# Kernel optimization log

Hardware: AMD Instinct MI355X
Metric: run time of the kernel (lower is better)

Reference implementation:

```python
import jax, jax.numpy as jnp
import numpy as np

DT = 600.0          # init kwarg: dt (seconds)
STEPS = 48          # init kwarg: steps
R_EARTH = 6371000.0
DEG2RAD = np.pi / 180.0


def setup_inputs() -> dict:
    key = jax.random.key(0)
    k1, k2, k3 = jax.random.split(key, 3)
    B, H, W = 8, 1024, 1024
    T = jax.random.normal(k1, (B, H, W), jnp.float32)
    ug = 0.5 * jax.random.normal(k2, (B, H, W), jnp.float32)
    vg = 0.5 * jax.random.normal(k3, (B, H, W), jnp.float32)
    lat = jnp.linspace(20.0, 60.0, H, dtype=jnp.float32)   # degrees, matches repo linspace(20,60,nx)
    lon = jnp.linspace(100.0, 150.0, W, dtype=jnp.float32)  # degrees, matches repo linspace(100,150,ny)
    mask = jnp.ones((H, W), jnp.float32)
    return {"T": T, "ug": ug, "vg": vg, "lat": lat, "lon": lon, "mask": mask}


def reference(T, ug, vg, lat, lon, mask):
    dtype = T.dtype
    dlat = lat[1] - lat[0]
    dlon = lon[1] - lon[0]
    dy = R_EARTH * DEG2RAD * dlat                        # scalar
    # dx depends only on latitude (row): shape (H,1) -> broadcast (1,H,1)
    dx = (R_EARTH * DEG2RAD * dlon) * jnp.cos(lat * DEG2RAD)[:, None]
    dx_b = dx[None]                                       # (1,H,1)
    m = mask[None]                                        # (1,H,W)
    kernel = (jnp.array([[1., 2., 1.], [2., 4., 2.], [1., 2., 1.]], dtype) / 16.0).reshape(1, 1, 3, 3)

    def deriv_y(Tc):  # centered interior, one-sided edges along H (axis 1)
        mid = (Tc[:, 2:] - Tc[:, :-2]) / (2.0 * dy)
        top = (Tc[:, 1:2] - Tc[:, 0:1]) / dy
        bot = (Tc[:, -1:] - Tc[:, -2:-1]) / dy
        return jnp.concatenate([top, mid, bot], axis=1)

    def deriv_x(Tc):  # centered interior, one-sided edges along W (axis 2); dx is W-independent
        mid = (Tc[:, :, 2:] - Tc[:, :, :-2]) / (2.0 * dx_b)
        left = (Tc[:, :, 1:2] - Tc[:, :, 0:1]) / dx_b
        right = (Tc[:, :, -1:] - Tc[:, :, -2:-1]) / dx_b
        return jnp.concatenate([left, mid, right], axis=2)

    def smooth(x):  # 3x3 binomial filter, SAME (zero) padding, then mask
        y = jax.lax.conv_general_dilated(
            x[:, None], kernel, window_strides=(1, 1), padding=((1, 1), (1, 1)),
            dimension_numbers=("NCHW", "OIHW", "NCHW"))
        return y[:, 0] * m

    def step(Tc, _):
        Fc = -(ug * deriv_x(Tc) + vg * deriv_y(Tc)) * m   # masked advective tendency
        Tn = smooth(Tc + DT * Fc)
        return Tn, None

    T_final, _ = jax.lax.scan(step, T, None, length=STEPS)
    return T_final
```

## Files before the change

kernel.cpp:

```cpp
#include <hip/hip_runtime.h>


#define DEG2RAD 0.017453292519943295f
#define R_EARTH 6371000.0f
#define DT_S 600.0f

constexpr int NT    = 256;
constexpr int STRIP = 8;
constexpr int WPW   = 256;

__global__ __launch_bounds__(256)
void prep_kernel(const float* __restrict__ lat, const float* __restrict__ lon,
                 float* __restrict__ coef, int H) {
    int h = blockIdx.x * blockDim.x + threadIdx.x;
    if (h < H) {
        float dlon = lon[1] - lon[0];
        coef[h] = 1.0f / (R_EARTH * DEG2RAD * dlon * cosf(lat[h] * DEG2RAD));
    }
    if (h == 0) {
        float dlat = lat[1] - lat[0];
        coef[H] = 1.0f / (R_EARTH * DEG2RAD * dlat);
    }
}

constexpr int FWAVES = 4;
constexpr int SH3    = 8;
constexpr int NITER3 = SH3 + 10;

__global__ __launch_bounds__(256, 2)
void fused3_kernel(const float* __restrict__ Tin, const float* __restrict__ ug,
                   const float* __restrict__ vg, const float* __restrict__ mask,
                   const float* __restrict__ coef, float* __restrict__ Tout,
                   int H, int W) {
    const int lane = threadIdx.x & 63;
    const int wv   = threadIdx.x >> 6;
    const int h0   = blockIdx.x * SH3;
    const int b    = blockIdx.y;
    const int gw   = (wv << 8) + (lane << 2);
    const size_t plane = (size_t)H * W;
    const float* __restrict__ Tb  = Tin + b * plane;
    const float* __restrict__ ugb = ug  + b * plane;
    const float* __restrict__ vgb = vg  + b * plane;
    float* __restrict__ To = Tout + b * plane;
    const float inv_dy = coef[H];
    const bool isL = (lane == 0), isR = (lane == 63);
    const bool domL = (wv == 0), domR = (wv == FWAVES - 1);

    __shared__ float eT [8][FWAVES][2];
    __shared__ float eA1[8][FWAVES][2];
    __shared__ float eS1[8][FWAVES][2];
    __shared__ float eA2[8][FWAVES][2];
    __shared__ float eS2[8][FWAVES][2];
    __shared__ float eA3[8][FWAVES][2];

    auto rowc = [&](int r) { return min(max(r, 0), H - 1); };
    auto ld4 = [&](const float* __restrict__ p, int r) -> float4 {
        return *(const float4*)(p + (size_t)rowc(r) * W + gw);
    };
    const float4 z4 = make_float4(0.f, 0.f, 0.f, 0.f);

    float4 t0 = z4;
    float4 t1 = ld4(Tb, h0 - 6);
    float4 t2 = ld4(Tb, h0 - 5);
    float4 t3 = ld4(Tb, h0 - 4);
    float4 u0 = ld4(ugb, h0 - 5), u1 = z4, u2 = z4, u3 = z4, u4 = z4, u5 = z4;
    float4 g0 = ld4(vgb, h0 - 5), g1 = z4, g2 = z4, g3 = z4, g4 = z4, g5 = z4;
    float4 m0 = ld4(mask, h0 - 5), m1 = z4, m2 = z4, m3 = z4, m4 = z4, m5 = z4, m6 = z4;
    float4 a1p = z4, a1c = z4, a1n = z4;
    float4 s1p = z4, s1c = z4, s1n = z4;
    float4 a2p = z4, a2c = z4, a2n = z4;
    float4 s2p = z4, s2c = z4, s2n = z4;
    float4 a3p = z4, a3c = z4, a3n = z4;

    if (isL) { eT[3][wv][0] = t2.x; eT[4][wv][0] = t3.x; }
    if (isR) { eT[3][wv][1] = t2.w; eT[4][wv][1] = t3.w; }
    asm volatile("s_waitcnt lgkmcnt(0)" ::: "memory");
    __builtin_amdgcn_s_barrier();

    #pragma unroll
    for (int j = 0; j < NITER3; ++j) {
        const int a = h0 - 5 + j;
        const int rg_a1p = (j + 4) & 7;
        const int rg_a   = (j + 3) & 7;
        const int rg_am1 = (j + 2) & 7;
        const int rg_am2 = (j + 1) & 7;
        const int rg_am3 = (j + 0) & 7;
        const int rg_am4 = (j + 7) & 7;
        const int rg_am5 = (j + 6) & 7;
        const int rg_am6 = (j + 5) & 7;

        t0 = t1; t1 = t2; t2 = t3; t3 = ld4(Tb, a + 2);
        u5 = u4; u4 = u3; u3 = u2; u2 = u1; u1 = u0; u0 = ld4(ugb, a + 1);
        g5 = g4; g4 = g3; g3 = g2; g2 = g1; g1 = g0; g0 = ld4(vgb, a + 1);
        m6 = m5; m5 = m4; m4 = m3; m3 = m2; m2 = m1; m1 = m0; m0 = ld4(mask, a + 1);

        if (isL) eT[rg_a1p][wv][0] = t2.x;
        if (isR) eT[rg_a1p][wv][1] = t2.w;

        float4 a1_new = z4;
        if (a >= 0 && a < H) {
            const float ix  = coef[a];
            const float sy  = (a == 0 || a == H - 1) ? inv_dy : 0.5f * inv_dy;
            const float sxh = 0.5f * ix;
            float cL = __shfl_up(t1.w, 1);
            float cR = __shfl_down(t1.x, 1);
            float sxx = sxh, sxw = sxh;
            if (isL) { if (domL) { cL = t1.x; sxx = ix; } else cL = eT[rg_a][wv - 1][1]; }
            if (isR) { if (domR) { cR = t1.w; sxw = ix; } else cR = eT[rg_a][wv + 1][0]; }
            a1_new.x = t1.x + DT_S * (-(u1.x * ((t1.y - cL ) * sxx) + g1.x * ((t2.x - t0.x) * sy)) * m1.x);
            a1_new.y = t1.y + DT_S * (-(u1.y * ((t1.z - t1.x) * sxh) + g1.y * ((t2.y - t0.y) * sy)) * m1.y);
            a1_new.z = t1.z + DT_S * (-(u1.z * ((t1.w - t1.y) * sxh) + g1.z * ((t2.z - t0.z) * sy)) * m1.z);
            a1_new.w = t1.w + DT_S * (-(u1.w * ((cR  - t1.z) * sxw) + g1.w * ((t2.w - t0.w) * sy)) * m1.w);
        }
        if (isL) eA1[rg_a][wv][0] = a1_new.x;
        if (isR) eA1[rg_a][wv][1] = a1_new.w;
        a1n = a1_new;

        asm volatile("s_waitcnt lgkmcnt(0)" ::: "memory");
        __builtin_amdgcn_s_barrier();

        float4 s1_new = z4;
        if (j >= 2) {
            const int s = a - 1;
            if (s >= 0 && s < H) {
                float4 v;
                v.x = a1p.x + 2.f * a1c.x + a1n.x;
                v.y = a1p.y + 2.f * a1c.y + a1n.y;
                v.z = a1p.z + 2.f * a1c.z + a1n.z;
                v.w = a1p.w + 2.f * a1c.w + a1n.w;
                float vL = __shfl_up(v.w, 1);
                float vR = __shfl_down(v.x, 1);
                if (isL) vL = domL ? 0.f
                    : (eA1[rg_am2][wv - 1][1] + 2.f * eA1[rg_am1][wv - 1][1] + eA1[rg_a][wv - 1][1]);
                if (isR) vR = domR ? 0.f
                    : (eA1[rg_am2][wv + 1][0] + 2.f * eA1[rg_am1][wv + 1][0] + eA1[rg_a][wv + 1][0]);
                s1_new.x = (vL  + 2.f * v.x + v.y) * 0.0625f * m2.x;
                s1_new.y = (v.x + 2.f * v.y + v.z) * 0.0625f * m2.y;
                s1_new.z = (v.y + 2.f * v.z + v.w) * 0.0625f * m2.z;
                s1_new.w = (v.z + 2.f * v.w + vR ) * 0.0625f * m2.w;
            }
            if (isL) eS1[rg_am1][wv][0] = s1_new.x;
            if (isR) eS1[rg_am1][wv][1] = s1_new.w;
        }
        a1p = a1c; a1c = a1n;
        s1n = s1_new;

        float4 a2_new = z4;
        if (j >= 4) {
            const int q = a - 2;
            if (q >= 0 && q < H) {
                const float ix  = coef[q];
                const float sxh = 0.5f * ix;
                float cL = __shfl_up(s1c.w, 1);
                float cR = __shfl_down(s1c.x, 1);
                float sxx = sxh, sxw = sxh;
                if (isL) { if (domL) { cL = s1c.x; sxx = ix; } else cL = eS1[rg_am2][wv - 1][1]; }
                if (isR) { if (domR) { cR = s1c.w; sxw = ix; } else cR = eS1[rg_am2][wv + 1][0]; }
                const float4 yl = (q == 0)     ? s1c : s1p;
                const float4 yh = (q == H - 1) ? s1c : s1n;
                const float sy  = (q == 0 || q == H - 1) ? inv_dy : 0.5f * inv_dy;
                a2_new.x = s1c.x + DT_S * (-(u3.x * ((s1c.y - cL  ) * sxx) + g3.x * ((yh.x - yl.x) * sy)) * m3.x);
                a2_new.y = s1c.y + DT_S * (-(u3.y * ((s1c.z - s1c.x) * sxh) + g3.y * ((yh.y - yl.y) * sy)) * m3.y);
                a2_new.z = s1c.z + DT_S * (-(u3.z * ((s1c.w - s1c.y) * sxh) + g3.z * ((yh.z - yl.z) * sy)) * m3.z);
                a2_new.w = s1c.w + DT_S * (-(u3.w * ((cR   - s1c.z) * sxw) + g3.w * ((yh.w - yl.w) * sy)) * m3.w);
            }
            if (isL) eA2[rg_am2][wv][0] = a2_new.x;
            if (isR) eA2[rg_am2][wv][1] = a2_new.w;
        }
        s1p = s1c; s1c = s1n;
        a2n = a2_new;

        asm volatile("s_waitcnt lgkmcnt(0)" ::: "memory");
        __builtin_amdgcn_s_barrier();

        float4 s2_new = z4;
        if (j >= 6) {
            const int s = a - 3;
            if (s >= 0 && s < H) {
                float4 v;
                v.x = a2p.x + 2.f * a2c.x + a2n.x;
                v.y = a2p.y + 2.f * a2c.y + a2n.y;
                v.z = a2p.z + 2.f * a2c.z + a2n.z;
                v.w = a2p.w + 2.f * a2c.w + a2n.w;
                float vL = __shfl_up(v.w, 1);
                float vR = __shfl_down(v.x, 1);
                if (isL) vL = domL ? 0.f
                    : (eA2[rg_am4][wv - 1][1] + 2.f * eA2[rg_am3][wv - 1][1] + eA2[rg_am2][wv - 1][1]);
                if (isR) vR = domR ? 0.f
                    : (eA2[rg_am4][wv + 1][0] + 2.f * eA2[rg_am3][wv + 1][0] + eA2[rg_am2][wv + 1][0]);
                s2_new.x = (vL  + 2.f * v.x + v.y) * 0.0625f * m4.x;
                s2_new.y = (v.x + 2.f * v.y + v.z) * 0.0625f * m4.y;
                s2_new.z = (v.y + 2.f * v.z + v.w) * 0.0625f * m4.z;
                s2_new.w = (v.z + 2.f * v.w + vR ) * 0.0625f * m4.w;
            }
            if (isL) eS2[rg_am3][wv][0] = s2_new.x;
            if (isR) eS2[rg_am3][wv][1] = s2_new.w;
        }
        a2p = a2c; a2c = a2n;
        s2n = s2_new;

        float4 a3_new = z4;
        if (j >= 8) {
            const int p = a - 4;
            if (p >= 0 && p < H) {
                const float ix  = coef[p];
                const float sxh = 0.5f * ix;
                float cL = __shfl_up(s2c.w, 1);
                float cR = __shfl_down(s2c.x, 1);
                float sxx = sxh, sxw = sxh;
                if (isL) { if (domL) { cL = s2c.x; sxx = ix; } else cL = eS2[rg_am4][wv - 1][1]; }
                if (isR) { if (domR) { cR = s2c.w; sxw = ix; } else cR = eS2[rg_am4][wv + 1][0]; }
                const float4 yl = (p == 0)     ? s2c : s2p;
                const float4 yh = (p == H - 1) ? s2c : s2n;
                const float sy  = (p == 0 || p == H - 1) ? inv_dy : 0.5f * inv_dy;
                a3_new.x = s2c.x + DT_S * (-(u5.x * ((s2c.y - cL  ) * sxx) + g5.x * ((yh.x - yl.x) * sy)) * m5.x);
                a3_new.y = s2c.y + DT_S * (-(u5.y * ((s2c.z - s2c.x) * sxh) + g5.y * ((yh.y - yl.y) * sy)) * m5.y);
                a3_new.z = s2c.z + DT_S * (-(u5.z * ((s2c.w - s2c.y) * sxh) + g5.z * ((yh.z - yl.z) * sy)) * m5.z);
                a3_new.w = s2c.w + DT_S * (-(u5.w * ((cR   - s2c.z) * sxw) + g5.w * ((yh.w - yl.w) * sy)) * m5.w);
            }
            if (isL) eA3[rg_am4][wv][0] = a3_new.x;
            if (isR) eA3[rg_am4][wv][1] = a3_new.w;
        }
        s2p = s2c; s2c = s2n;
        a3n = a3_new;

        asm volatile("s_waitcnt lgkmcnt(0)" ::: "memory");
        __builtin_amdgcn_s_barrier();

        if (j >= 10) {
            const int r = a - 5;
            if (r < H) {
                float4 v;
                v.x = a3p.x + 2.f * a3c.x + a3n.x;
                v.y = a3p.y + 2.f * a3c.y + a3n.y;
                v.z = a3p.z + 2.f * a3c.z + a3n.z;
                v.w = a3p.w + 2.f * a3c.w + a3n.w;
                float vL = __shfl_up(v.w, 1);
                float vR = __shfl_down(v.x, 1);
                if (isL) vL = domL ? 0.f
                    : (eA3[rg_am6][wv - 1][1] + 2.f * eA3[rg_am5][wv - 1][1] + eA3[rg_am4][wv - 1][1]);
                if (isR) vR = domR ? 0.f
                    : (eA3[rg_am6][wv + 1][0] + 2.f * eA3[rg_am5][wv + 1][0] + eA3[rg_am4][wv + 1][0]);
                float4 o;
                o.x = (vL  + 2.f * v.x + v.y) * 0.0625f * m6.x;
                o.y = (v.x + 2.f * v.y + v.z) * 0.0625f * m6.y;
                o.z = (v.y + 2.f * v.z + v.w) * 0.0625f * m6.z;
                o.w = (v.z + 2.f * v.w + vR ) * 0.0625f * m6.w;
                *(float4*)(To + (size_t)r * W + gw) = o;
            }
        }
        a3p = a3c; a3c = a3n;
    }
}

__global__ __launch_bounds__(256, 4)
void stream_kernel(const float* __restrict__ Tin, const float* __restrict__ ug,
                   const float* __restrict__ vg, const float* __restrict__ mask,
                   const float* __restrict__ coef, float* __restrict__ Tout,
                   int H, int W) {
    const int lane = threadIdx.x & 63;
    const int wv   = threadIdx.x >> 6;
    const int ws   = blockIdx.x * WPW;
    const int hs   = (blockIdx.y * 4 + wv) * STRIP;
    const int b    = blockIdx.z;
    if (hs >= H) return;
    const size_t plane = (size_t)H * W;
    const float* __restrict__ Tb  = Tin + b * plane;
    const float* __restrict__ ugb = ug  + b * plane;
    const float* __restrict__ vgb = vg  + b * plane;
    float* __restrict__ To = Tout + b * plane;
    const float inv_dy = coef[H];
    const bool atL = (ws == 0);
    const bool atR = (ws + WPW >= W);
    const bool isL = (lane == 0);
    const bool isR = (lane == 63);
    const int gw = ws + 4 * lane;

    auto clampr = [&](int r) { return min(max(r, 0), H - 1); };
    auto ldT = [&](int r) -> float4 {
        return *(const float4*)(Tb + (size_t)clampr(r) * W + gw);
    };
    auto ldL = [&](int r) -> float2 {
        float4 q = *(const float4*)(Tb + (size_t)clampr(r) * W + (ws - 4));
        return make_float2(q.z, q.w);
    };
    auto ldR = [&](int r) -> float2 {
        float4 q = *(const float4*)(Tb + (size_t)clampr(r) * W + (ws + WPW));
        return make_float2(q.x, q.y);
    };

    float4 tp, tc, tn;
    float  tLp_w = 0.f; float2 tLc = make_float2(0.f, 0.f), tLn = make_float2(0.f, 0.f);
    float  tRp_x = 0.f; float2 tRc = make_float2(0.f, 0.f), tRn = make_float2(0.f, 0.f);

    auto roll = [&](int rnext) {
        tp = tc; tc = tn; tn = ldT(rnext);
        if (!atL) { tLp_w = tLc.y; tLc = tLn; tLn = ldL(rnext); }
        if (!atR) { tRp_x = tRc.x; tRc = tRn; tRn = ldR(rnext); }
    };

    auto advrow = [&](int r, float4& a, float& aL, float& aR, float4& mOut) {
        if (r < 0 || r >= H) {
            a = make_float4(0.f, 0.f, 0.f, 0.f); aL = 0.f; aR = 0.f;
            mOut = make_float4(0.f, 0.f, 0.f, 0.f); return;
        }
        const size_t ro = (size_t)r * W;
        const float ix  = coef[r];
        const float sy  = (r == 0 || r == H - 1) ? inv_dy : 0.5f * inv_dy;
        const float sxh = 0.5f * ix;
        float4 u4 = *(const float4*)(ugb + ro + gw);
        float4 g4 = *(const float4*)(vgb + ro + gw);
        float4 m4 = *(const float4*)(mask + ro + gw);
        float cLw = __shfl_up(tc.w, 1);
        float cRx = __shfl_down(tc.x, 1);
        float sxx = sxh, sxw = sxh;
        if (isL) { if (atL) { cLw = tc.x; sxx = ix; } else { cLw = tLc.y; } }
        if (isR) { if (atR) { cRx = tc.w; sxw = ix; } else { cRx = tRc.x; } }
        a.x = tc.x + DT_S * (-(u4.x * ((tc.y - cLw) * sxx) + g4.x * ((tn.x - tp.x) * sy)) * m4.x);
        a.y = tc.y + DT_S * (-(u4.y * ((tc.z - tc.x) * sxh) + g4.y * ((tn.y - tp.y) * sy)) * m4.y);
        a.z = tc.z + DT_S * (-(u4.z * ((tc.w - tc.y) * sxh) + g4.z * ((tn.z - tp.z) * sy)) * m4.z);
        a.w = tc.w + DT_S * (-(u4.w * ((cRx - tc.z) * sxw) + g4.w * ((tn.w - tp.w) * sy)) * m4.w);
        if (!atL) {
            float uL = ((const float4*)(ugb + ro + (ws - 4)))->w;
            float gL = ((const float4*)(vgb + ro + (ws - 4)))->w;
            float mL = ((const float4*)(mask + ro + (ws - 4)))->w;
            aL = tLc.y + DT_S * (-(uL * ((tc.x - tLc.x) * sxh) + gL * ((tLn.y - tLp_w) * sy)) * mL);
        } else aL = 0.f;
        if (!atR) {
            float uR = ((const float4*)(ugb + ro + (ws + WPW)))->x;
            float gR = ((const float4*)(vgb + ro + (ws + WPW)))->x;
            float mR = ((const float4*)(mask + ro + (ws + WPW)))->x;
            aR = tRc.x + DT_S * (-(uR * ((tRc.y - tc.w) * sxh) + gR * ((tRn.x - tRp_x) * sy)) * mR);
        } else aR = 0.f;
        mOut = m4;
    };

    tp = ldT(hs - 2); tc = ldT(hs - 1); tn = ldT(hs);
    if (!atL) { float2 q = ldL(hs - 2); tLp_w = q.y; tLc = ldL(hs - 1); tLn = ldL(hs); }
    if (!atR) { float2 q = ldR(hs - 2); tRp_x = q.x; tRc = ldR(hs - 1); tRn = ldR(hs); }

    float4 ap, ac, an, mC, mN, mdum;
    float aLp, aLc, aLn, aRp, aRc, aRn;
    advrow(hs - 1, ap, aLp, aRp, mdum);
    roll(hs + 1);
    advrow(hs, ac, aLc, aRc, mC);

    #pragma unroll
    for (int i = 0; i < STRIP; ++i) {
        const int go = hs + i;
        roll(go + 2);
        advrow(go + 1, an, aLn, aRn, mN);
        if (go < H) {
            float4 v;
            v.x = ap.x + 2.f * ac.x + an.x;
            v.y = ap.y + 2.f * ac.y + an.y;
            v.z = ap.z + 2.f * ac.z + an.z;
            v.w = ap.w + 2.f * ac.w + an.w;
            float vL  = aLp + 2.f * aLc + aLn;
            float vR  = aRp + 2.f * aRc + aRn;
            float vLw = __shfl_up(v.w, 1);
            float vRx = __shfl_down(v.x, 1);
            if (isL) vLw = atL ? 0.f : vL;
            if (isR) vRx = atR ? 0.f : vR;
            float4 o;
            o.x = (vLw + 2.f * v.x + v.y) * 0.0625f * mC.x;
            o.y = (v.x + 2.f * v.y + v.z) * 0.0625f * mC.y;
            o.z = (v.y + 2.f * v.z + v.w) * 0.0625f * mC.z;
            o.w = (v.z + 2.f * v.w + vRx) * 0.0625f * mC.w;
            *(float4*)(To + (size_t)go * W + gw) = o;
        }
        ap = ac; ac = an;
        aLp = aLc; aLc = aLn; aRp = aRc; aRc = aRn;
        mC = mN;
    }
}

constexpr int FTW = 64, FTH = 32;
constexpr int FSTW = FTW + 4, FSTH = FTH + 4;
constexpr int FMTW = FTW + 2, FMTH = FTH + 2;

__global__ __launch_bounds__(256)
void step_tile(const float* __restrict__ Tin, const float* __restrict__ ug,
               const float* __restrict__ vg, const float* __restrict__ mask,
               const float* __restrict__ coef, float* __restrict__ Tout,
               int H, int W) {
    __shared__ float sT[FSTH][FSTW];
    __shared__ float sM[FMTH][FMTW];
    const int tid = threadIdx.x;
    const int w0 = blockIdx.x * FTW;
    const int h0 = blockIdx.y * FTH;
    const int b  = blockIdx.z;
    const long plane = (long)H * W;
    const float* Tb  = Tin + b * plane;
    const float* ugb = ug  + b * plane;
    const float* vgb = vg  + b * plane;
    const float inv_dy = coef[H];

    for (int i = tid; i < FSTH * FSTW; i += NT) {
        int r = i / FSTW, c = i - r * FSTW;
        int gh = min(max(h0 - 2 + r, 0), H - 1);
        int gw = min(max(w0 - 2 + c, 0), W - 1);
        sT[r][c] = Tb[gh * W + gw];
    }
    __syncthreads();
    for (int i = tid; i < FMTH * FMTW; i += NT) {
        int r = i / FMTW, c = i - r * FMTW;
        int gh = h0 - 1 + r, gw = w0 - 1 + c;
        float v = 0.0f;
        if (gh >= 0 && gh < H && gw >= 0 && gw < W) {
            int sr = r + 1, sc = c + 1;
            float ndy = sT[sr + 1][sc] - sT[sr - 1][sc];
            float ndx = sT[sr][sc + 1] - sT[sr][sc - 1];
            float sy  = (gh == 0 || gh == H - 1) ? inv_dy : 0.5f * inv_dy;
            float ix  = coef[gh];
            float sx  = (gw == 0 || gw == W - 1) ? ix : 0.5f * ix;
            int   gi  = gh * W + gw;
            float F   = -(ugb[gi] * (ndx * sx) + vgb[gi] * (ndy * sy)) * mask[gi];
            v = sT[sr][sc] + DT_S * F;
        }
        sM[r][c] = v;
    }
    __syncthreads();
    float* To = Tout + b * plane;
    for (int i = tid; i < FTH * FTW; i += NT) {
        int r = i >> 6, c = i & (FTW - 1);
        int gh = h0 + r, gw = w0 + c;
        if (gh < H && gw < W) {
            int sr = r + 1, sc = c + 1;
            float s = (sM[sr-1][sc-1] + sM[sr-1][sc+1] + sM[sr+1][sc-1] + sM[sr+1][sc+1])
                    + 2.0f * (sM[sr-1][sc] + sM[sr+1][sc] + sM[sr][sc-1] + sM[sr][sc+1])
                    + 4.0f * sM[sr][sc];
            To[gh * W + gw] = s * 0.0625f * mask[gh * W + gw];
        }
    }
}

extern "C" void kernel_launch(void* const* d_in, const int* in_sizes, int n_in,
                              void* d_out, int out_size, void* d_ws, size_t ws_size,
                              hipStream_t stream) {
    const float* T0   = (const float*)d_in[0];
    const float* ug   = (const float*)d_in[1];
    const float* vg   = (const float*)d_in[2];
    const float* lat  = (const float*)d_in[3];
    const float* lon  = (const float*)d_in[4];
    const float* mask = (const float*)d_in[5];

    const int H = in_sizes[3];
    const int W = in_sizes[4];
    const int B = in_sizes[0] / (H * W);

    float* out  = (float*)d_out;
    float* ping = (float*)d_ws;
    float* coef = ping + (size_t)B * H * W;

    prep_kernel<<<dim3((H + NT - 1) / NT), dim3(NT), 0, stream>>>(lat, lon, coef, H);

    const int STEPS = 48;

    if (W == FWAVES * 256) {
        dim3 gridF3((H + SH3 - 1) / SH3, B);
        const int NLAUNCH = STEPS / 3;
        for (int i = 0; i < NLAUNCH; ++i) {
            const float* src = (i == 0) ? T0 : ((i & 1) ? ping : out);
            float*       dst = (i & 1) ? out : ping;
            fused3_kernel<<<gridF3, dim3(NT), 0, stream>>>(src, ug, vg, mask, coef, dst, H, W);
        }
    } else {
        const bool fast = (W % WPW) == 0;
        dim3 gridS(W / (fast ? WPW : 1), (H + 4 * STRIP - 1) / (4 * STRIP), B);
        dim3 gridF((W + FTW - 1) / FTW, (H + FTH - 1) / FTH, B);
        for (int i = 0; i < STEPS; ++i) {
            const float* src = (i == 0) ? T0 : ((i & 1) ? ping : out);
            float*       dst = (i & 1) ? out : ping;
            if (fast)
                stream_kernel<<<gridS, dim3(NT), 0, stream>>>(src, ug, vg, mask, coef, dst, H, W);
            else
                step_tile<<<gridF, dim3(NT), 0, stream>>>(src, ug, vg, mask, coef, dst, H, W);
        }
    }
}
```

Before: 1.090 ms.

## Fuse four timesteps per launch with taller row strips

The temporal-blocking kernel now advances four advection+smoothing steps per launch instead of three, and each block processes 16 output rows instead of 8. This cuts the number of launches and full-field reads and writes of T, ug, vg and mask per step, and the taller strip amortises the recomputed halo rows. In exchange it raises register pressure from the extra pipeline stages and rolling buffers, adds more barriers per iteration, and leaves fewer blocks in the grid.

```diff
diff --git a/kernel.cpp b/kernel.cpp
--- a/kernel.cpp
+++ b/kernel.cpp
@@ -24,17 +24,17 @@
 }
 
 constexpr int FWAVES = 4;
-constexpr int SH3    = 8;
-constexpr int NITER3 = SH3 + 10;
+constexpr int SH4    = 16;
+constexpr int NITER4 = SH4 + 14;
 
 __global__ __launch_bounds__(256, 2)
-void fused3_kernel(const float* __restrict__ Tin, const float* __restrict__ ug,
+void fused4_kernel(const float* __restrict__ Tin, const float* __restrict__ ug,
                    const float* __restrict__ vg, const float* __restrict__ mask,
                    const float* __restrict__ coef, float* __restrict__ Tout,
                    int H, int W) {
     const int lane = threadIdx.x & 63;
     const int wv   = threadIdx.x >> 6;
-    const int h0   = blockIdx.x * SH3;
+    const int h0   = blockIdx.x * SH4;
     const int b    = blockIdx.y;
     const int gw   = (wv << 8) + (lane << 2);
     const size_t plane = (size_t)H * W;
@@ -52,6 +52,8 @@
     __shared__ float eA2[8][FWAVES][2];
     __shared__ float eS2[8][FWAVES][2];
     __shared__ float eA3[8][FWAVES][2];
+    __shared__ float eS3[8][FWAVES][2];
+    __shared__ float eA4[8][FWAVES][2];
 
     auto rowc = [&](int r) { return min(max(r, 0), H - 1); };
     auto ld4 = [&](const float* __restrict__ p, int r) -> float4 {
@@ -60,42 +62,46 @@
     const float4 z4 = make_float4(0.f, 0.f, 0.f, 0.f);
 
     float4 t0 = z4;
-    float4 t1 = ld4(Tb, h0 - 6);
-    float4 t2 = ld4(Tb, h0 - 5);
-    float4 t3 = ld4(Tb, h0 - 4);
-    float4 u0 = ld4(ugb, h0 - 5), u1 = z4, u2 = z4, u3 = z4, u4 = z4, u5 = z4;
-    float4 g0 = ld4(vgb, h0 - 5), g1 = z4, g2 = z4, g3 = z4, g4 = z4, g5 = z4;
-    float4 m0 = ld4(mask, h0 - 5), m1 = z4, m2 = z4, m3 = z4, m4 = z4, m5 = z4, m6 = z4;
+    float4 t1 = ld4(Tb, h0 - 8);
+    float4 t2 = ld4(Tb, h0 - 7);
+    float4 t3 = ld4(Tb, h0 - 6);
+    float4 u0 = ld4(ugb, h0 - 7), u1 = z4, u2 = z4, u3 = z4, u4 = z4, u5 = z4, u6 = z4, u7 = z4;
+    float4 g0 = ld4(vgb, h0 - 7), g1 = z4, g2 = z4, g3 = z4, g4 = z4, g5 = z4, g6 = z4, g7 = z4;
+    float4 m0 = ld4(mask, h0 - 7), m1 = z4, m2 = z4, m3 = z4, m4 = z4, m5 = z4, m6 = z4, m7 = z4, m8 = z4;
     float4 a1p = z4, a1c = z4, a1n = z4;
     float4 s1p = z4, s1c = z4, s1n = z4;
     float4 a2p = z4, a2c = z4, a2n = z4;
     float4 s2p = z4, s2c = z4, s2n = z4;
     float4 a3p = z4, a3c = z4, a3n = z4;
-
-    if (isL) { eT[3][wv][0] = t2.x; eT[4][wv][0] = t3.x; }
-    if (isR) { eT[3][wv][1] = t2.w; eT[4][wv][1] = t3.w; }
+    float4 s3p = z4, s3c = z4, s3n = z4;
+    float4 a4p = z4, a4c = z4, a4n = z4;
+
+    if (isL) { eT[1][wv][0] = t2.x; eT[2][wv][0] = t3.x; }
+    if (isR) { eT[1][wv][1] = t2.w; eT[2][wv][1] = t3.w; }
     asm volatile("s_waitcnt lgkmcnt(0)" ::: "memory");
     __builtin_amdgcn_s_barrier();
 
     #pragma unroll
-    for (int j = 0; j < NITER3; ++j) {
-        const int a = h0 - 5 + j;
-        const int rg_a1p = (j + 4) & 7;
-        const int rg_a   = (j + 3) & 7;
-        const int rg_am1 = (j + 2) & 7;
-        const int rg_am2 = (j + 1) & 7;
-        const int rg_am3 = (j + 0) & 7;
-        const int rg_am4 = (j + 7) & 7;
-        const int rg_am5 = (j + 6) & 7;
-        const int rg_am6 = (j + 5) & 7;
+    for (int j = 0; j < NITER4; ++j) {
+        const int a = h0 - 7 + j;
+        const int sl_a1p = (j + 2) & 7;
+        const int sl_a   = (j + 1) & 7;
+        const int sl_m1  = (j + 0) & 7;
+        const int sl_m2  = (j + 7) & 7;
+        const int sl_m3  = (j + 6) & 7;
+        const int sl_m4  = (j + 5) & 7;
+        const int sl_m5  = (j + 4) & 7;
+        const int sl_m6  = (j + 3) & 7;
+        const int sl_m7  = (j + 2) & 7;
+        const int sl_m8  = (j + 1) & 7;
 
         t0 = t1; t1 = t2; t2 = t3; t3 = ld4(Tb, a + 2);
-        u5 = u4; u4 = u3; u3 = u2; u2 = u1; u1 = u0; u0 = ld4(ugb, a + 1);
-        g5 = g4; g4 = g3; g3 = g2; g2 = g1; g1 = g0; g0 = ld4(vgb, a + 1);
-        m6 = m5; m5 = m4; m4 = m3; m3 = m2; m2 = m1; m1 = m0; m0 = ld4(mask, a + 1);
-
-        if (isL) eT[rg_a1p][wv][0] = t2.x;
-        if (isR) eT[rg_a1p][wv][1] = t2.w;
+        u7 = u6; u6 = u5; u5 = u4; u4 = u3; u3 = u2; u2 = u1; u1 = u0; u0 = ld4(ugb, a + 1);
+        g7 = g6; g6 = g5; g5 = g4; g4 = g3; g3 = g2; g2 = g1; g1 = g0; g0 = ld4(vgb, a + 1);
+        m8 = m7; m7 = m6; m6 = m5; m5 = m4; m4 = m3; m3 = m2; m2 = m1; m1 = m0; m0 = ld4(mask, a + 1);
+
+        if (isL) eT[sl_a1p][wv][0] = t2.x;
+        if (isR) eT[sl_a1p][wv][1] = t2.w;
 
         float4 a1_new = z4;
         if (a >= 0 && a < H) {
@@ -105,15 +111,15 @@
             float cL = __shfl_up(t1.w, 1);
             float cR = __shfl_down(t1.x, 1);
             float sxx = sxh, sxw = sxh;
-            if (isL) { if (domL) { cL = t1.x; sxx = ix; } else cL = eT[rg_a][wv - 1][1]; }
-            if (isR) { if (domR) { cR = t1.w; sxw = ix; } else cR = eT[rg_a][wv + 1][0]; }
+            if (isL) { if (domL) { cL = t1.x; sxx = ix; } else cL = eT[sl_a][wv - 1][1]; }
+            if (isR) { if (domR) { cR = t1.w; sxw = ix; } else cR = eT[sl_a][wv + 1][0]; }
             a1_new.x = t1.x + DT_S * (-(u1.x * ((t1.y - cL ) * sxx) + g1.x * ((t2.x - t0.x) * sy)) * m1.x);
             a1_new.y = t1.y + DT_S * (-(u1.y * ((t1.z - t1.x) * sxh) + g1.y * ((t2.y - t0.y) * sy)) * m1.y);
             a1_new.z = t1.z + DT_S * (-(u1.z * ((t1.w - t1.y) * sxh) + g1.z * ((t2.z - t0.z) * sy)) * m1.z);
             a1_new.w = t1.w + DT_S * (-(u1.w * ((cR  - t1.z) * sxw) + g1.w * ((t2.w - t0.w) * sy)) * m1.w);
         }
-        if (isL) eA1[rg_a][wv][0] = a1_new.x;
-        if (isR) eA1[rg_a][wv][1] = a1_new.w;
+        if (isL) eA1[sl_a][wv][0] = a1_new.x;
+        if (isR) eA1[sl_a][wv][1] = a1_new.w;
         a1n = a1_new;
 
         asm volatile("s_waitcnt lgkmcnt(0)" ::: "memory");
@@ -131,16 +137,16 @@
                 float vL = __shfl_up(v.w, 1);
                 float vR = __shfl_down(v.x, 1);
                 if (isL) vL = domL ? 0.f
-                    : (eA1[rg_am2][wv - 1][1] + 2.f * eA1[rg_am1][wv - 1][1] + eA1[rg_a][wv - 1][1]);
+                    : (eA1[sl_m2][wv - 1][1] + 2.f * eA1[sl_m1][wv - 1][1] + eA1[sl_a][wv - 1][1]);
                 if (isR) vR = domR ? 0.f
-                    : (eA1[rg_am2][wv + 1][0] + 2.f * eA1[rg_am1][wv + 1][0] + eA1[rg_a][wv + 1][0]);
+                    : (eA1[sl_m2][wv + 1][0] + 2.f * eA1[sl_m1][wv + 1][0] + eA1[sl_a][wv + 1][0]);
                 s1_new.x = (vL  + 2.f * v.x + v.y) * 0.0625f * m2.x;
                 s1_new.y = (v.x + 2.f * v.y + v.z) * 0.0625f * m2.y;
                 s1_new.z = (v.y + 2.f * v.z + v.w) * 0.0625f * m2.z;
                 s1_new.w = (v.z + 2.f * v.w + vR ) * 0.0625f * m2.w;
             }
-            if (isL) eS1[rg_am1][wv][0] = s1_new.x;
-            if (isR) eS1[rg_am1][wv][1] = s1_new.w;
+            if (isL) eS1[sl_m1][wv][0] = s1_new.x;
+            if (isR) eS1[sl_m1][wv][1] = s1_new.w;
         }
         a1p = a1c; a1c = a1n;
         s1n = s1_new;
@@ -154,8 +160,8 @@
                 float cL = __shfl_up(s1c.w, 1);
                 float cR = __shfl_down(s1c.x, 1);
                 float sxx = sxh, sxw = sxh;
-                if (isL) { if (domL) { cL = s1c.x; sxx = ix; } else cL = eS1[rg_am2][wv - 1][1]; }
-                if (isR) { if (domR) { cR = s1c.w; sxw = ix; } else cR = eS1[rg_am2][wv + 1][0]; }
+                if (isL) { if (domL) { cL = s1c.x; sxx = ix; } else cL = eS1[sl_m2][wv - 1][1]; }
+                if (isR) { if (domR) { cR = s1c.w; sxw = ix; } else cR = eS1[sl_m2][wv + 1][0]; }
                 const float4 yl = (q == 0)     ? s1c : s1p;
                 const float4 yh = (q == H - 1) ? s1c : s1n;
                 const float sy  = (q == 0 || q == H - 1) ? inv_dy : 0.5f * inv_dy;
@@ -164,8 +170,8 @@
                 a2_new.z = s1c.z + DT_S * (-(u3.z * ((s1c.w - s1c.y) * sxh) + g3.z * ((yh.z - yl.z) * sy)) * m3.z);
                 a2_new.w = s1c.w + DT_S * (-(u3.w * ((cR   - s1c.z) * sxw) + g3.w * ((yh.w - yl.w) * sy)) * m3.w);
             }
-            if (isL) eA2[rg_am2][wv][0] = a2_new.x;
-            if (isR) eA2[rg_am2][wv][1] = a2_new.w;
+            if (isL) eA2[sl_m2][wv][0] = a2_new.x;
+            if (isR) eA2[sl_m2][wv][1] = a2_new.w;
         }
         s1p = s1c; s1c = s1n;
         a2n = a2_new;
@@ -185,16 +191,16 @@
                 float vL = __shfl_up(v.w, 1);
                 float vR = __shfl_down(v.x, 1);
                 if (isL) vL = domL ? 0.f
-                    : (eA2[rg_am4][wv - 1][1] + 2.f * eA2[rg_am3][wv - 1][1] + eA2[rg_am2][wv - 1][1]);
+                    : (eA2[sl_m4][wv - 1][1] + 2.f * eA2[sl_m3][wv - 1][1] + eA2[sl_m2][wv - 1][1]);
                 if (isR) vR = domR ? 0.f
-                    : (eA2[rg_am4][wv + 1][0] + 2.f * eA2[rg_am3][wv + 1][0] + eA2[rg_am2][wv + 1][0]);
+                    : (eA2[sl_m4][wv + 1][0] + 2.f * eA2[sl_m3][wv + 1][0] + eA2[sl_m2][wv + 1][0]);
                 s2_new.x = (vL  + 2.f * v.x + v.y) * 0.0625f * m4.x;
                 s2_new.y = (v.x + 2.f * v.y + v.z) * 0.0625f * m4.y;
                 s2_new.z = (v.y + 2.f * v.z + v.w) * 0.0625f * m4.z;
                 s2_new.w = (v.z + 2.f * v.w + vR ) * 0.0625f * m4.w;
             }
-            if (isL) eS2[rg_am3][wv][0] = s2_new.x;
-            if (isR) eS2[rg_am3][wv][1] = s2_new.w;
+            if (isL) eS2[sl_m3][wv][0] = s2_new.x;
+            if (isR) eS2[sl_m3][wv][1] = s2_new.w;
         }
         a2p = a2c; a2c = a2n;
         s2n = s2_new;
@@ -208,8 +214,8 @@
                 float cL = __shfl_up(s2c.w, 1);
                 float cR = __shfl_down(s2c.x, 1);
                 float sxx = sxh, sxw = sxh;
-                if (isL) { if (domL) { cL = s2c.x; sxx = ix; } else cL = eS2[rg_am4][wv - 1][1]; }
-                if (isR) { if (domR) { cR = s2c.w; sxw = ix; } else cR = eS2[rg_am4][wv + 1][0]; }
+                if (isL) { if (domL) { cL = s2c.x; sxx = ix; } else cL = eS2[sl_m4][wv - 1][1]; }
+                if (isR) { if (domR) { cR = s2c.w; sxw = ix; } else cR = eS2[sl_m4][wv + 1][0]; }
                 const float4 yl = (p == 0)     ? s2c : s2p;
                 const float4 yh = (p == H - 1) ? s2c : s2n;
                 const float sy  = (p == 0 || p == H - 1) ? inv_dy : 0.5f * inv_dy;
@@ -218,8 +224,8 @@
                 a3_new.z = s2c.z + DT_S * (-(u5.z * ((s2c.w - s2c.y) * sxh) + g5.z * ((yh.z - yl.z) * sy)) * m5.z);
                 a3_new.w = s2c.w + DT_S * (-(u5.w * ((cR   - s2c.z) * sxw) + g5.w * ((yh.w - yl.w) * sy)) * m5.w);
             }
-            if (isL) eA3[rg_am4][wv][0] = a3_new.x;
-            if (isR) eA3[rg_am4][wv][1] = a3_new.w;
+            if (isL) eA3[sl_m4][wv][0] = a3_new.x;
+            if (isR) eA3[sl_m4][wv][1] = a3_new.w;
         }
         s2p = s2c; s2c = s2n;
         a3n = a3_new;
@@ -227,9 +233,10 @@
         asm volatile("s_waitcnt lgkmcnt(0)" ::: "memory");
         __builtin_amdgcn_s_barrier();
 
+        float4 s3_new = z4;
         if (j >= 10) {
-            const int r = a - 5;
-            if (r < H) {
+            const int s = a - 5;
+            if (s >= 0 && s < H) {
                 float4 v;
                 v.x = a3p.x + 2.f * a3c.x + a3n.x;
                 v.y = a3p.y + 2.f * a3c.y + a3n.y;
@@ -238,18 +245,71 @@
                 float vL = __shfl_up(v.w, 1);
                 float vR = __shfl_down(v.x, 1);
                 if (isL) vL = domL ? 0.f
-                    : (eA3[rg_am6][wv - 1][1] + 2.f * eA3[rg_am5][wv - 1][1] + eA3[rg_am4][wv - 1][1]);
+                    : (eA3[sl_m6][wv - 1][1] + 2.f * eA3[sl_m5][wv - 1][1] + eA3[sl_m4][wv - 1][1]);
                 if (isR) vR = domR ? 0.f
-                    : (eA3[rg_am6][wv + 1][0] + 2.f * eA3[rg_am5][wv + 1][0] + eA3[rg_am4][wv + 1][0]);
+                    : (eA3[sl_m6][wv + 1][0] + 2.f * eA3[sl_m5][wv + 1][0] + eA3[sl_m4][wv + 1][0]);
+                s3_new.x = (vL  + 2.f * v.x + v.y) * 0.0625f * m6.x;
+                s3_new.y = (v.x + 2.f * v.y + v.z) * 0.0625f * m6.y;
+                s3_new.z = (v.y + 2.f * v.z + v.w) * 0.0625f * m6.z;
+                s3_new.w = (v.z + 2.f * v.w + vR ) * 0.0625f * m6.w;
+            }
+            if (isL) eS3[sl_m5][wv][0] = s3_new.x;
+            if (isR) eS3[sl_m5][wv][1] = s3_new.w;
+        }
+        a3p = a3c; a3c = a3n;
+        s3n = s3_new;
+
+        float4 a4_new = z4;
+        if (j >= 12) {
+            const int p = a - 6;
+            if (p >= 0 && p < H) {
+                const float ix  = coef[p];
+                const float sxh = 0.5f * ix;
+                float cL = __shfl_up(s3c.w, 1);
+                float cR = __shfl_down(s3c.x, 1);
+                float sxx = sxh, sxw = sxh;
+                if (isL) { if (domL) { cL = s3c.x; sxx = ix; } else cL = eS3[sl_m6][wv - 1][1]; }
+                if (isR) { if (domR) { cR = s3c.w; sxw = ix; } else cR = eS3[sl_m6][wv + 1][0]; }
+                const float4 yl = (p == 0)     ? s3c : s3p;
+                const float4 yh = (p == H - 1) ? s3c : s3n;
+                const float sy  = (p == 0 || p == H - 1) ? inv_dy : 0.5f * inv_dy;
+                a4_new.x = s3c.x + DT_S * (-(u7.x * ((s3c.y - cL  ) * sxx) + g7.x * ((yh.x - yl.x) * sy)) * m7.x);
+                a4_new.y = s3c.y + DT_S * (-(u7.y * ((s3c.z - s3c.x) * sxh) + g7.y * ((yh.y - yl.y) * sy)) * m7.y);
+                a4_new.z = s3c.z + DT_S * (-(u7.z * ((s3c.w - s3c.y) * sxh) + g7.z * ((yh.z - yl.z) * sy)) * m7.z);
+                a4_new.w = s3c.w + DT_S * (-(u7.w * ((cR   - s3c.z) * sxw) + g7.w * ((yh.w - yl.w) * sy)) * m7.w);
+            }
+            if (isL) eA4[sl_m6][wv][0] = a4_new.x;
+            if (isR) eA4[sl_m6][wv][1] = a4_new.w;
+        }
+        s3p = s3c; s3c = s3n;
+        a4n = a4_new;
+
+        asm volatile("s_waitcnt lgkmcnt(0)" ::: "memory");
+        __builtin_amdgcn_s_barrier();
+
+        if (j >= 14) {
+            const int r = a - 7;
+            if (r < H) {
+                float4 v;
+                v.x = a4p.x + 2.f * a4c.x + a4n.x;
+                v.y = a4p.y + 2.f * a4c.y + a4n.y;
+                v.z = a4p.z + 2.f * a4c.z + a4n.z;
+                v.w = a4p.w + 2.f * a4c.w + a4n.w;
+                float vL = __shfl_up(v.w, 1);
+                float vR = __shfl_down(v.x, 1);
+                if (isL) vL = domL ? 0.f
+                    : (eA4[sl_m8][wv - 1][1] + 2.f * eA4[sl_m7][wv - 1][1] + eA4[sl_m6][wv - 1][1]);
+                if (isR) vR = domR ? 0.f
+                    : (eA4[sl_m8][wv + 1][0] + 2.f * eA4[sl_m7][wv + 1][0] + eA4[sl_m6][wv + 1][0]);
                 float4 o;
-                o.x = (vL  + 2.f * v.x + v.y) * 0.0625f * m6.x;
-                o.y = (v.x + 2.f * v.y + v.z) * 0.0625f * m6.y;
-                o.z = (v.y + 2.f * v.z + v.w) * 0.0625f * m6.z;
-                o.w = (v.z + 2.f * v.w + vR ) * 0.0625f * m6.w;
+                o.x = (vL  + 2.f * v.x + v.y) * 0.0625f * m8.x;
+                o.y = (v.x + 2.f * v.y + v.z) * 0.0625f * m8.y;
+                o.z = (v.y + 2.f * v.z + v.w) * 0.0625f * m8.z;
+                o.w = (v.z + 2.f * v.w + vR ) * 0.0625f * m8.w;
                 *(float4*)(To + (size_t)r * W + gw) = o;
             }
         }
-        a3p = a3c; a3c = a3n;
+        a4p = a4c; a4c = a4n;
     }
 }
 
@@ -458,12 +518,12 @@
     const int STEPS = 48;
 
     if (W == FWAVES * 256) {
-        dim3 gridF3((H + SH3 - 1) / SH3, B);
-        const int NLAUNCH = STEPS / 3;
+        dim3 gridF4((H + SH4 - 1) / SH4, B);
+        const int NLAUNCH = STEPS / 4;
         for (int i = 0; i < NLAUNCH; ++i) {
             const float* src = (i == 0) ? T0 : ((i & 1) ? ping : out);
             float*       dst = (i & 1) ? out : ping;
-            fused3_kernel<<<gridF3, dim3(NT), 0, stream>>>(src, ug, vg, mask, coef, dst, H, W);
+            fused4_kernel<<<gridF4, dim3(NT), 0, stream>>>(src, ug, vg, mask, coef, dst, H, W);
         }
     } else {
         const bool fast = (W % WPW) == 0;
```

New measurement: 2.016 ms. 1.85x slower.
